# Kernel optimization log

Measured on AMD Instinct MI355X. Metric: run time of the kernel, lower is better.

Reference implementation:

```python
import jax, jax.numpy as jnp
import numpy as np

QLEN, KLEN, BSZ, NHEAD, DHEAD = 1024, 1024, 2, 16, 64
RLEN = QLEN + KLEN
SCALE = 1.0 / np.sqrt(DHEAD).astype(np.float32)  # 1/sqrt(d_head)


def setup_inputs() -> dict:
    key = jax.random.key(0)
    ks = jax.random.split(key, 10)
    return {
        "q_head": jax.random.normal(ks[0], (QLEN, BSZ, NHEAD, DHEAD), jnp.float32),
        "k_head_h": jax.random.normal(ks[1], (KLEN, BSZ, NHEAD, DHEAD), jnp.float32),
        "v_head_h": jax.random.normal(ks[2], (KLEN, BSZ, NHEAD, DHEAD), jnp.float32),
        "k_head_r": jax.random.normal(ks[3], (RLEN, BSZ, NHEAD, DHEAD), jnp.float32),
        "seg_embed": jax.random.normal(ks[4], (2, NHEAD, DHEAD), jnp.float32),
        "seg_mat": jax.random.uniform(ks[5], (QLEN, KLEN, BSZ, 2), jnp.float32),
        "r_w_bias": jax.random.normal(ks[6], (NHEAD, DHEAD), jnp.float32),
        "r_r_bias": jax.random.normal(ks[7], (NHEAD, DHEAD), jnp.float32),
        "r_s_bias": jax.random.normal(ks[8], (NHEAD, DHEAD), jnp.float32),
        "attn_mask": jnp.zeros((QLEN, KLEN, 1, 1), jnp.float32),
    }


def _rel_shift(x, klen):
    # x: [qlen, rlen, bsz, n_head] -> [qlen, klen, bsz, n_head]
    x = jnp.transpose(x, (1, 0, 2, 3))[1:]          # drop first position row
    x = jnp.transpose(x, (1, 0, 2, 3))[:, :klen]    # keep first klen columns
    return x


def reference(q_head, k_head_h, v_head_h, k_head_r, seg_embed, seg_mat,
              r_w_bias, r_r_bias, r_s_bias, attn_mask):
    # content-based score
    ac = jnp.einsum('ibnd,jbnd->ijbn', q_head + r_w_bias, k_head_h)
    # position-based score with relative shift
    bd = jnp.einsum('ibnd,jbnd->ijbn', q_head + r_r_bias, k_head_r)
    bd = _rel_shift(bd, klen=ac.shape[1])
    # segment-based score
    ef = jnp.einsum('ibnd,snd->ibns', q_head + r_s_bias, seg_embed)
    ef = jnp.einsum('ijbs,ibns->ijbn', seg_mat, ef)
    attn_score = (ac + bd + ef) * SCALE
    attn_score = attn_score - 1e30 * attn_mask
    attn_prob = jax.nn.softmax(attn_score, axis=1)  # over key dim j
    attn_vec = jnp.einsum('ijbn,jbnd->ibnd', attn_prob, v_head_h)
    return attn_vec
```

## Files before the change

### kernel.cpp

```cpp
#include <hip/hip_runtime.h>

#define QLEN 1024
#define KLEN 1024
#define BSZ 2
#define NHEAD 16
#define DHEAD 64
#define RS 2048
#define BLK_I 64
#define BLK_J 32
#define NT32 (KLEN / BLK_J)
#define NBN (BSZ * NHEAD)

#define SC2f  0.18033688011112440f
#define MBIGf 1.4426950408889634e30f
#define THRf  8.0f

#define SEGP_BYTES  16777216u
#define KT_BYTES    ((size_t)NBN * NT32 * 4096)
#define OPART_BYTES 16777216u
#define ML_BYTES    524288u

typedef __attribute__((ext_vector_type(8))) short s16x8;
typedef __attribute__((ext_vector_type(4))) short s16x4;
typedef __attribute__((ext_vector_type(8))) unsigned short u16x8;
typedef __attribute__((ext_vector_type(4))) unsigned short u16x4;
typedef __attribute__((ext_vector_type(4))) float f32x4;
typedef __attribute__((ext_vector_type(2))) float f32x2;

__device__ __forceinline__ unsigned short f2bf(float f) {
    union { float f; unsigned int u; } x; x.f = f;
    unsigned int r = x.u + 0x7fffu + ((x.u >> 16) & 1u);
    return (unsigned short)(r >> 16);
}
__device__ __forceinline__ float bf2f(unsigned short h) {
    union { unsigned int u; float f; } x; x.u = ((unsigned int)h) << 16;
    return x.f;
}

__device__ __forceinline__ f32x4 mfma16x16x16(s16x4 a, s16x4 b, f32x4 c) {
#if __has_builtin(__builtin_amdgcn_mfma_f32_16x16x16bf16_1k)
    return __builtin_amdgcn_mfma_f32_16x16x16bf16_1k(a, b, c, 0, 0, 0);
#else
    f32x4 d;
    asm("v_mfma_f32_16x16x16_bf16 %0, %1, %2, %3"
        : "=v"(d) : "v"(a), "v"(b), "0"(c));
    return d;
#endif
}

typedef const __attribute__((address_space(1))) unsigned int* gas_t;
typedef __attribute__((address_space(3))) unsigned int* las_t;
__device__ __forceinline__ void gl_lds16(const void* g, void* l) {
    __builtin_amdgcn_global_load_lds((gas_t)g, (las_t)l, 16, 0, 0);
}

__global__ __launch_bounds__(256)
void pack_all_kernel(const float* __restrict__ segmat,
                     const float* __restrict__ mask,
                     const float* __restrict__ kh,
                     const float* __restrict__ kr,
                     const float* __restrict__ v,
                     unsigned short* __restrict__ segT,
                     unsigned short* __restrict__ Kp,
                     unsigned short* __restrict__ Krp,
                     unsigned short* __restrict__ Vtp)
{
    __shared__ float smS[16][32][4];
    __shared__ float smM[16][33];
    __shared__ float VT[32][65];
    const int bid = blockIdx.x;
    const int tid = threadIdx.x;

    if (bid < 2048) {
        const int istrip = bid >> 5;
        const int jt     = bid & 31;
        const int ib     = istrip * 16;
        const int jb     = jt * 32;
        {
            const int il = tid >> 4;
            const int j2 = (tid & 15) * 2;
            const float* sp = segmat + ((size_t)(ib + il) * KLEN + jb + j2) * 4;
            *(f32x4*)&smS[il][j2][0]     = *(const f32x4*)sp;
            *(f32x4*)&smS[il][j2 + 1][0] = *(const f32x4*)(sp + 4);
            const float* mp = mask + (size_t)(ib + il) * KLEN + jb + j2;
            smM[il][j2]     = mp[0] * MBIGf;
            smM[il][j2 + 1] = mp[1] * MBIGf;
        }
        __syncthreads();
        const int k  = tid >> 6;
        const int l  = tid & 63;
        const int q4 = l >> 4;
        const int il = l & 15;
        const int jl = (k >> 1) * 16 + q4 * 4 + (k & 1) * 2;
#pragma unroll
        for (int b = 0; b < 2; ++b) {
            u16x8 o;
#pragma unroll
            for (int e = 0; e < 2; ++e) {
                o[e * 4 + 0] = f2bf(smS[il][jl + e][b * 2]);
                o[e * 4 + 1] = f2bf(smS[il][jl + e][b * 2 + 1]);
                o[e * 4 + 2] = f2bf(smM[il][jl + e]);
                o[e * 4 + 3] = 0;
            }
            unsigned short* op = segT + ((size_t)(b * 64 + istrip) << 16)
                                 + (jt << 11) + tid * 8;
            *(u16x8*)op = o;
        }
    } else {
        const int blk = bid - 2048;
        const int bn  = blk >> 5;
        const int jt  = blk & (NT32 - 1);
        const int b   = bn & 1;
        const int n   = bn >> 1;
        const int boff = b * NHEAD * DHEAD + n * DHEAD;
        const int j0  = jt * BLK_J;

        {
            const int j  = tid >> 3;
            const int dq = (tid & 7) * 8;
            const float* vp = v + (size_t)(j0 + j) * RS + boff + dq;
#pragma unroll
            for (int e = 0; e < 8; ++e) VT[j][dq + e] = vp[e];
        }
        __syncthreads();

        const size_t tb = (size_t)blk * 2048;
        {
            const int row = tid >> 3;
            const int ch  = (tid & 7) ^ (row & 7);
            u16x8 ok, orr;
            const float* hp = kh + (size_t)(j0 + row) * RS + boff + ch * 8;
            const float* rp = kr + (size_t)(j0 + row + 1) * RS + boff + ch * 8;
#pragma unroll
            for (int e = 0; e < 8; ++e) { ok[e] = f2bf(hp[e]); orr[e] = f2bf(rp[e]); }
            *(u16x8*)&Kp [tb + (size_t)tid * 8] = ok;
            *(u16x8*)&Krp[tb + (size_t)tid * 8] = orr;
        }
        {
            const int d  = tid >> 2;
            const int gl = tid & 3;
#pragma unroll
            for (int s = 0; s < 2; ++s) {
                const int gj8 = gl * 2 + s;
                const int ph  = gj8 ^ (d & 7);
                u16x4 ov;
#pragma unroll
                for (int e = 0; e < 4; ++e) ov[e] = f2bf(VT[gj8 * 4 + e][d]);
                *(u16x4*)&Vtp[tb + (size_t)d * 32 + ph * 4] = ov;
            }
        }
    }
}

__global__ __launch_bounds__(256)
void merge_kernel(const float* __restrict__ opart,
                  const float* __restrict__ ml,
                  float* __restrict__ out)
{
    const int gid = blockIdx.x * 256 + threadIdx.x;
    const int d   = gid & 63;
    const int rr  = gid >> 6;
    const int i   = rr & (QLEN - 1);
    const int n   = (rr >> 10) & (NHEAD - 1);
    const int b   = rr >> 14;
    const int r0  = rr;
    const int r1  = (NBN * QLEN) + rr;
    const float m0 = ml[r0 * 2], l0 = ml[r0 * 2 + 1];
    const float m1 = ml[r1 * 2], l1 = ml[r1 * 2 + 1];
    const float M  = fmaxf(m0, m1);
    const float w0 = __builtin_amdgcn_exp2f(m0 - M);
    const float w1 = __builtin_amdgcn_exp2f(m1 - M);
    const float inv = 1.f / (l0 * w0 + l1 * w1);
    const float o = (opart[(size_t)r0 * 64 + d] * w0 + opart[(size_t)r1 * 64 + d] * w1) * inv;
    out[(size_t)i * RS + b * NHEAD * DHEAD + n * DHEAD + d] = o;
}

__global__ __launch_bounds__(256, 4)
void relattn_kernel(const float* __restrict__ q,
                    const float* __restrict__ segemb,
                    const float* __restrict__ rwb,
                    const float* __restrict__ rrb,
                    const float* __restrict__ rsb,
                    const unsigned short* __restrict__ segT,
                    const unsigned short* __restrict__ Kp,
                    const unsigned short* __restrict__ Krp,
                    const unsigned short* __restrict__ Vtp,
                    float* __restrict__ opart,
                    float* __restrict__ mlpart,
                    float* __restrict__ out,
                    int jsplit, int njt)
{
    __shared__ unsigned short KhL[3][32][64];
    __shared__ unsigned short KrL[3][32][64];
    __shared__ unsigned short VtL[3][64][32];

    const int F = blockIdx.x;
    const int x = F & 7;
    const int k = F >> 3;
    const int g = (k >> 4) * 8 + x;
    const int n = k & 15;
    int i0, b, jsp;
    if (jsplit) { i0 = (g >> 2) * BLK_I; b = (g >> 1) & 1; jsp = g & 1; }
    else        { i0 = (g >> 1) * BLK_I; b = g & 1;        jsp = 0;    }
    const int bn = n * 2 + b;
    const int boff = b * NHEAD * DHEAD + n * DHEAD;

    const int tid  = threadIdx.x;
    const int wave = tid >> 6;
    const int lane = tid & 63;
    const int q4   = lane >> 4;
    const int c    = lane & 15;
    const int iRow = i0 + wave * 16 + c;

    s16x8 qwf[2], qrf[2];
    float e0, e1;
    {
        const float* qp = q + (size_t)iRow * RS + boff;
        float es0 = 0.f, es1 = 0.f;
#pragma unroll
        for (int kk = 0; kk < 2; ++kk) {
            const int off = kk * 32 + q4 * 8;
            const f32x4 q0 = *(const f32x4*)(qp + off);
            const f32x4 q1 = *(const f32x4*)(qp + off + 4);
            const f32x4 w0 = *(const f32x4*)(rwb + n * DHEAD + off);
            const f32x4 w1 = *(const f32x4*)(rwb + n * DHEAD + off + 4);
            const f32x4 r0 = *(const f32x4*)(rrb + n * DHEAD + off);
            const f32x4 r1 = *(const f32x4*)(rrb + n * DHEAD + off + 4);
            const f32x4 sa = *(const f32x4*)(segemb + n * DHEAD + off);
            const f32x4 sb = *(const f32x4*)(segemb + n * DHEAD + off + 4);
            const f32x4 ta = *(const f32x4*)(segemb + (NHEAD + n) * DHEAD + off);
            const f32x4 tb = *(const f32x4*)(segemb + (NHEAD + n) * DHEAD + off + 4);
            const f32x4 ra = *(const f32x4*)(rsb + n * DHEAD + off);
            const f32x4 rb = *(const f32x4*)(rsb + n * DHEAD + off + 4);
            s16x8 tw, tr;
#pragma unroll
            for (int e = 0; e < 4; ++e) {
                tw[e]     = (short)f2bf((q0[e] + w0[e]) * SC2f);
                tw[4 + e] = (short)f2bf((q1[e] + w1[e]) * SC2f);
                tr[e]     = (short)f2bf((q0[e] + r0[e]) * SC2f);
                tr[4 + e] = (short)f2bf((q1[e] + r1[e]) * SC2f);
                es0 += (q0[e] + ra[e]) * sa[e] + (q1[e] + rb[e]) * sb[e];
                es1 += (q0[e] + ra[e]) * ta[e] + (q1[e] + rb[e]) * tb[e];
            }
            qwf[kk] = tw; qrf[kk] = tr;
        }
        es0 += __shfl_xor(es0, 16, 64); es0 += __shfl_xor(es0, 32, 64);
        es1 += __shfl_xor(es1, 16, 64); es1 += __shfl_xor(es1, 32, 64);
        e0 = es0 * SC2f; e1 = es1 * SC2f;
    }

    const int tbase = bn * NT32 + jsp * njt;
    auto stage = [&](int jt, int buf) {
        const size_t toff = ((size_t)(tbase + jt)) << 12;
        const int go = tid * 16;
        const int lo = wave * 1024;
        gl_lds16((const char*)Kp  + toff + go, (char*)&KhL[buf][0][0] + lo);
        gl_lds16((const char*)Krp + toff + go, (char*)&KrL[buf][0][0] + lo);
        gl_lds16((const char*)Vtp + toff + go, (char*)&VtL[buf][0][0] + lo);
    };
    const unsigned short* segW = segT + ((size_t)(b * 64 + (i0 >> 4) + wave) << 16);
    auto segload = [&](int jt, u16x8 (&pg)[4]) {
        const unsigned short* st = segW + ((jsp * njt + jt) << 11);
        pg[0] = *(const u16x8*)(st + lane * 8);
        pg[1] = *(const u16x8*)(st + 512 + lane * 8);
        pg[2] = *(const u16x8*)(st + 1024 + lane * 8);
        pg[3] = *(const u16x8*)(st + 1536 + lane * 8);
    };

    float m = -INFINITY, lsum = 0.f;
    f32x4 acc[4];
#pragma unroll
    for (int dt = 0; dt < 4; ++dt) acc[dt] = (f32x4)0.f;

    u16x8 pgA[4], pgB[4];
    stage(0, 0);
    __builtin_amdgcn_sched_barrier(0);
    segload(0, pgA);
    __builtin_amdgcn_sched_barrier(0);
    stage(1, 1);
    __builtin_amdgcn_sched_barrier(0);
    asm volatile("s_waitcnt vmcnt(7)" ::: "memory");
    __builtin_amdgcn_s_barrier();
    __builtin_amdgcn_sched_barrier(0);

    int cur = 0;
    auto body = [&](int t, u16x8 (&pgC)[4], u16x8 (&pgN)[4]) {
        const int tn1 = (t + 1 < njt) ? t + 1 : njt - 1;
        const int tn2 = (t + 2 < njt) ? t + 2 : njt - 1;
        int b2 = cur + 2; if (b2 >= 3) b2 -= 3;
        segload(tn1, pgN);
        __builtin_amdgcn_sched_barrier(0);
        stage(tn2, b2);
        __builtin_amdgcn_sched_barrier(0);

        f32x4 sjT[2];
        sjT[0] = (f32x4)0.f; sjT[1] = (f32x4)0.f;
        __builtin_amdgcn_s_setprio(1);
#pragma unroll
        for (int kk = 0; kk < 2; ++kk)
#pragma unroll
            for (int js = 0; js < 2; ++js) {
                const int row = js * 16 + c;
                const int pcK = ((kk * 4 + q4) ^ (c & 7)) * 8;
                const s16x8 khf = *(const s16x8*)&KhL[cur][row][pcK];
                const s16x8 krf = *(const s16x8*)&KrL[cur][row][pcK];
                sjT[js] = __builtin_amdgcn_mfma_f32_16x16x32_bf16(khf, qwf[kk], sjT[js], 0, 0, 0);
                sjT[js] = __builtin_amdgcn_mfma_f32_16x16x32_bf16(krf, qrf[kk], sjT[js], 0, 0, 0);
            }
        __builtin_amdgcn_s_setprio(0);

        float sc8[8];
#pragma unroll
        for (int js = 0; js < 2; ++js)
#pragma unroll
            for (int r = 0; r < 4; ++r) {
                const u16x8 g2 = pgC[js * 2 + (r >> 1)];
                const int bb = (r & 1) * 4;
                sc8[js * 4 + r] = sjT[js][r]
                                  + bf2f(g2[bb]) * e0 + bf2f(g2[bb + 1]) * e1
                                  - bf2f(g2[bb + 2]);
            }
        float pmax = fmaxf(
            fmaxf(fmaxf(sc8[0], sc8[1]), fmaxf(sc8[2], sc8[3])),
            fmaxf(fmaxf(sc8[4], sc8[5]), fmaxf(sc8[6], sc8[7])));

        if (!__all(pmax <= m + THRf)) {
            float mt = pmax;
            mt = fmaxf(mt, __shfl_xor(mt, 16, 64));
            mt = fmaxf(mt, __shfl_xor(mt, 32, 64));
            const float mn  = fmaxf(m, mt);
            const float scl = __builtin_amdgcn_exp2f(m - mn);
            m = mn;
            lsum *= scl;
#pragma unroll
            for (int dt = 0; dt < 4; ++dt) acc[dt] *= scl;
        }

        float p[8], ps = 0.f;
#pragma unroll
        for (int e = 0; e < 8; ++e) {
            p[e] = __builtin_amdgcn_exp2f(sc8[e] - m);
            ps += p[e];
        }
        lsum += ps;

        s16x4 pf4[2];
#pragma unroll
        for (int js = 0; js < 2; ++js) {
            union { unsigned int w[2]; s16x4 v; } pk2;
            asm("v_cvt_pk_bf16_f32 %0, %1, %2" : "=v"(pk2.w[0]) : "v"(p[js*4+0]), "v"(p[js*4+1]));
            asm("v_cvt_pk_bf16_f32 %0, %1, %2" : "=v"(pk2.w[1]) : "v"(p[js*4+2]), "v"(p[js*4+3]));
            pf4[js] = pk2.v;
        }
        __builtin_amdgcn_s_setprio(1);
#pragma unroll
        for (int dt = 0; dt < 4; ++dt) {
            const unsigned short* vrow = &VtL[cur][dt * 16 + c][0];
#pragma unroll
            for (int js = 0; js < 2; ++js) {
                const int ph = (js * 4 + q4) ^ (c & 7);
                const s16x4 vf = *(const s16x4*)(vrow + ph * 4);
                acc[dt] = mfma16x16x16(vf, pf4[js], acc[dt]);
            }
        }
        __builtin_amdgcn_s_setprio(0);

        asm volatile("s_waitcnt vmcnt(3)" ::: "memory");
        __builtin_amdgcn_s_barrier();
        __builtin_amdgcn_sched_barrier(0);
        ++cur; if (cur >= 3) cur = 0;
    };

    for (int o = 0; o < njt / 2; ++o) {
        body(2 * o + 0, pgA, pgB);
        body(2 * o + 1, pgB, pgA);
    }
    asm volatile("s_waitcnt vmcnt(0)" ::: "memory");

    lsum += __shfl_xor(lsum, 16, 64);
    lsum += __shfl_xor(lsum, 32, 64);

    if (jsplit) {
        const int rowG = ((jsp * BSZ + b) * NHEAD + n) * QLEN + iRow;
#pragma unroll
        for (int dt = 0; dt < 4; ++dt)
            *(f32x4*)&opart[(size_t)rowG * 64 + dt * 16 + q4 * 4] = acc[dt];
        if (q4 == 0) {
            mlpart[(size_t)rowG * 2]     = m;
            mlpart[(size_t)rowG * 2 + 1] = lsum;
        }
    } else {
        const float inv = 1.f / lsum;
        float* op = out + (size_t)iRow * RS + boff;
#pragma unroll
        for (int dt = 0; dt < 4; ++dt) {
            const f32x4 o = acc[dt] * inv;
            *(f32x4*)&op[dt * 16 + q4 * 4] = o;
        }
    }
}

extern "C" void kernel_launch(void* const* d_in, const int* in_sizes, int n_in,
                              void* d_out, int out_size, void* d_ws, size_t ws_size,
                              hipStream_t stream) {
    const float* q   = (const float*)d_in[0];
    const float* kh  = (const float*)d_in[1];
    const float* v   = (const float*)d_in[2];
    const float* kr  = (const float*)d_in[3];
    const float* se  = (const float*)d_in[4];
    const float* sm  = (const float*)d_in[5];
    const float* rwb = (const float*)d_in[6];
    const float* rrb = (const float*)d_in[7];
    const float* rsb = (const float*)d_in[8];
    const float* msk = (const float*)d_in[9];
    float* out = (float*)d_out;

    char* wsb = (char*)d_ws;
    unsigned short* segT = (unsigned short*)wsb;
    unsigned short* Kp   = (unsigned short*)(wsb + SEGP_BYTES);
    unsigned short* Krp  = (unsigned short*)(wsb + SEGP_BYTES + KT_BYTES);
    unsigned short* Vtp  = (unsigned short*)(wsb + SEGP_BYTES + 2 * KT_BYTES);
    float* opart  = (float*)(wsb + SEGP_BYTES + 3 * KT_BYTES);
    float* mlpart = (float*)(wsb + SEGP_BYTES + 3 * KT_BYTES + OPART_BYTES);

    const int jsplit = (ws_size >= (size_t)SEGP_BYTES + 3 * KT_BYTES + OPART_BYTES + ML_BYTES) ? 1 : 0;
    const int njt    = jsplit ? NT32 / 2 : NT32;

    pack_all_kernel<<<2048 + NBN * NT32, 256, 0, stream>>>(sm, msk, kh, kr, v,
                                                           segT, Kp, Krp, Vtp);
    relattn_kernel<<<jsplit ? 1024 : 512, 256, 0, stream>>>(q, se, rwb, rrb, rsb,
                                                            segT, Kp, Krp, Vtp,
                                                            opart, mlpart, out,
                                                            jsplit, njt);
    if (jsplit)
        merge_kernel<<<NBN * QLEN * DHEAD / 256, 256, 0, stream>>>(opart, mlpart, out);
}
```

Before: 59.50 us.

## Simplify to double-buffered pipeline and store split partial outputs as bf16

The hand-scheduled triple-buffered LDS pipeline, with its explicit vmcnt waits, sched barriers and segment-mask prefetch one tile ahead, is replaced by a plain double-buffered loop. That loop prefetches only the next K/Kr/V tile, loads the segment data synchronously and uses __syncthreads. Partial outputs from the split-K path are now written and read as bf16, which halves opart traffic and makes the workspace requirement smaller. The trade-off is less latency hiding for global loads, plus extra rounding error in the partial accumulators before the merge.

New measurement: 57.22 us. 1.04x faster.

```diff
diff --git a/kernel.cpp b/kernel.cpp
--- a/kernel.cpp
+++ b/kernel.cpp
@@ -17,7 +17,7 @@
 
 #define SEGP_BYTES  16777216u
 #define KT_BYTES    ((size_t)NBN * NT32 * 4096)
-#define OPART_BYTES 16777216u
+#define OPART_BYTES 8388608u
 #define ML_BYTES    524288u
 
 typedef __attribute__((ext_vector_type(8))) short s16x8;
@@ -153,7 +153,7 @@
 }
 
 __global__ __launch_bounds__(256)
-void merge_kernel(const float* __restrict__ opart,
+void merge_kernel(const unsigned short* __restrict__ opart,
                   const float* __restrict__ ml,
                   float* __restrict__ out)
 {
@@ -171,7 +171,8 @@
     const float w0 = __builtin_amdgcn_exp2f(m0 - M);
     const float w1 = __builtin_amdgcn_exp2f(m1 - M);
     const float inv = 1.f / (l0 * w0 + l1 * w1);
-    const float o = (opart[(size_t)r0 * 64 + d] * w0 + opart[(size_t)r1 * 64 + d] * w1) * inv;
+    const float o = (bf2f(opart[(size_t)r0 * 64 + d]) * w0
+                   + bf2f(opart[(size_t)r1 * 64 + d]) * w1) * inv;
     out[(size_t)i * RS + b * NHEAD * DHEAD + n * DHEAD + d] = o;
 }
 
@@ -185,14 +186,14 @@
                     const unsigned short* __restrict__ Kp,
                     const unsigned short* __restrict__ Krp,
                     const unsigned short* __restrict__ Vtp,
-                    float* __restrict__ opart,
+                    unsigned short* __restrict__ opart,
                     float* __restrict__ mlpart,
                     float* __restrict__ out,
                     int jsplit, int njt)
 {
-    __shared__ unsigned short KhL[3][32][64];
-    __shared__ unsigned short KrL[3][32][64];
-    __shared__ unsigned short VtL[3][64][32];
+    __shared__ unsigned short KhL[2][32][64];
+    __shared__ unsigned short KrL[2][32][64];
+    __shared__ unsigned short VtL[2][64][32];
 
     const int F = blockIdx.x;
     const int x = F & 7;
@@ -258,40 +259,27 @@
         gl_lds16((const char*)Krp + toff + go, (char*)&KrL[buf][0][0] + lo);
         gl_lds16((const char*)Vtp + toff + go, (char*)&VtL[buf][0][0] + lo);
     };
+
+    stage(0, 0);
+    __syncthreads();
+
+    float m = -INFINITY, lsum = 0.f;
+    f32x4 acc[4];
+#pragma unroll
+    for (int dt = 0; dt < 4; ++dt) acc[dt] = (f32x4)0.f;
+
     const unsigned short* segW = segT + ((size_t)(b * 64 + (i0 >> 4) + wave) << 16);
-    auto segload = [&](int jt, u16x8 (&pg)[4]) {
+
+    int cur = 0;
+    for (int jt = 0; jt < njt; ++jt) {
+        if (jt + 1 < njt) stage(jt + 1, cur ^ 1);
+
         const unsigned short* st = segW + ((jsp * njt + jt) << 11);
+        u16x8 pg[4];
         pg[0] = *(const u16x8*)(st + lane * 8);
         pg[1] = *(const u16x8*)(st + 512 + lane * 8);
         pg[2] = *(const u16x8*)(st + 1024 + lane * 8);
         pg[3] = *(const u16x8*)(st + 1536 + lane * 8);
-    };
-
-    float m = -INFINITY, lsum = 0.f;
-    f32x4 acc[4];
-#pragma unroll
-    for (int dt = 0; dt < 4; ++dt) acc[dt] = (f32x4)0.f;
-
-    u16x8 pgA[4], pgB[4];
-    stage(0, 0);
-    __builtin_amdgcn_sched_barrier(0);
-    segload(0, pgA);
-    __builtin_amdgcn_sched_barrier(0);
-    stage(1, 1);
-    __builtin_amdgcn_sched_barrier(0);
-    asm volatile("s_waitcnt vmcnt(7)" ::: "memory");
-    __builtin_amdgcn_s_barrier();
-    __builtin_amdgcn_sched_barrier(0);
-
-    int cur = 0;
-    auto body = [&](int t, u16x8 (&pgC)[4], u16x8 (&pgN)[4]) {
-        const int tn1 = (t + 1 < njt) ? t + 1 : njt - 1;
-        const int tn2 = (t + 2 < njt) ? t + 2 : njt - 1;
-        int b2 = cur + 2; if (b2 >= 3) b2 -= 3;
-        segload(tn1, pgN);
-        __builtin_amdgcn_sched_barrier(0);
-        stage(tn2, b2);
-        __builtin_amdgcn_sched_barrier(0);
 
         f32x4 sjT[2];
         sjT[0] = (f32x4)0.f; sjT[1] = (f32x4)0.f;
@@ -314,7 +302,7 @@
         for (int js = 0; js < 2; ++js)
 #pragma unroll
             for (int r = 0; r < 4; ++r) {
-                const u16x8 g2 = pgC[js * 2 + (r >> 1)];
+                const u16x8 g2 = pg[js * 2 + (r >> 1)];
                 const int bb = (r & 1) * 4;
                 sc8[js * 4 + r] = sjT[js][r]
                                   + bf2f(g2[bb]) * e0 + bf2f(g2[bb + 1]) * e1
@@ -365,17 +353,9 @@
         }
         __builtin_amdgcn_s_setprio(0);
 
-        asm volatile("s_waitcnt vmcnt(3)" ::: "memory");
-        __builtin_amdgcn_s_barrier();
-        __builtin_amdgcn_sched_barrier(0);
-        ++cur; if (cur >= 3) cur = 0;
-    };
-
-    for (int o = 0; o < njt / 2; ++o) {
-        body(2 * o + 0, pgA, pgB);
-        body(2 * o + 1, pgB, pgA);
+        __syncthreads();
+        cur ^= 1;
     }
-    asm volatile("s_waitcnt vmcnt(0)" ::: "memory");
 
     lsum += __shfl_xor(lsum, 16, 64);
     lsum += __shfl_xor(lsum, 32, 64);
@@ -383,8 +363,12 @@
     if (jsplit) {
         const int rowG = ((jsp * BSZ + b) * NHEAD + n) * QLEN + iRow;
 #pragma unroll
-        for (int dt = 0; dt < 4; ++dt)
-            *(f32x4*)&opart[(size_t)rowG * 64 + dt * 16 + q4 * 4] = acc[dt];
+        for (int dt = 0; dt < 4; ++dt) {
+            u16x4 ob;
+#pragma unroll
+            for (int e = 0; e < 4; ++e) ob[e] = f2bf(acc[dt][e]);
+            *(u16x4*)&opart[(size_t)rowG * 64 + dt * 16 + q4 * 4] = ob;
+        }
         if (q4 == 0) {
             mlpart[(size_t)rowG * 2]     = m;
             mlpart[(size_t)rowG * 2 + 1] = lsum;
@@ -420,7 +404,7 @@
     unsigned short* Kp   = (unsigned short*)(wsb + SEGP_BYTES);
     unsigned short* Krp  = (unsigned short*)(wsb + SEGP_BYTES + KT_BYTES);
     unsigned short* Vtp  = (unsigned short*)(wsb + SEGP_BYTES + 2 * KT_BYTES);
-    float* opart  = (float*)(wsb + SEGP_BYTES + 3 * KT_BYTES);
+    unsigned short* opart = (unsigned short*)(wsb + SEGP_BYTES + 3 * KT_BYTES);
     float* mlpart = (float*)(wsb + SEGP_BYTES + 3 * KT_BYTES + OPART_BYTES);
 
     const int jsplit = (ws_size >= (size_t)SEGP_BYTES + 3 * KT_BYTES + OPART_BYTES + ML_BYTES) ? 1 : 0;
```
